# Performance work log

Hardware: AMD Instinct MI355X
Metric: run time of the kernel (lower is better)

Reference implementation:

```python
import jax, jax.numpy as jnp
import numpy as np

HID, HEADS = 2048, 16
HD = HID // HEADS  # head_dim = 128
EPS = 1e-6


def rope_tables(head_dim, max_pos, base=10000.0):
    inv = 1.0 / (base ** (jnp.arange(0, head_dim, 2, dtype=jnp.float32) / head_dim))
    t = jnp.arange(max_pos, dtype=jnp.float32)
    freqs = jnp.outer(t, inv)                      # [max_pos, d/2]
    emb = jnp.concatenate([freqs, freqs], axis=-1)  # [max_pos, d]
    return jnp.cos(emb), jnp.sin(emb)


def rotate_half(x):
    x1, x2 = jnp.split(x, 2, axis=-1)
    return jnp.concatenate([-x2, x1], axis=-1)


def lf_gate(x, c1w, c1b, c2w, c2b, rms_w):
    # x: [b, s, h]; prompt phase -> lf1/lf2 caches are zeros -> zero-pad 1 step on time axis
    xt = jnp.transpose(x, (0, 2, 1))[..., None]                 # [b, h, s, 1]
    xt = jnp.pad(xt, ((0, 0), (0, 0), (1, 0), (0, 0)))           # [b, h, s+1, 1]
    dn = ('NCHW', 'OIHW', 'NCHW')
    o1 = jax.lax.conv_general_dilated(xt, c1w, (1, 1), 'VALID', dimension_numbers=dn)
    o1 = o1 + c1b[None, :, None, None]                           # [b, h/2, s, 1]
    o1 = jnp.pad(o1, ((0, 0), (0, 0), (1, 0), (0, 0)))           # [b, h/2, s+1, 1]
    o2 = jax.lax.conv_general_dilated(o1, c2w, (1, 1), 'VALID', dimension_numbers=dn)
    o2 = o2 + c2b[None, :, None, None]                           # [b, h, s, 1]
    y = jnp.transpose(o2[..., 0], (0, 2, 1)) + x                 # residual, [b, s, h]
    var = jnp.mean(y * y, axis=-1, keepdims=True)
    return y * jax.lax.rsqrt(var + EPS) * rms_w


def setup_inputs() -> dict:
    key = jax.random.key(0)
    ks = jax.random.split(key, 10)
    b, s = 2, 2048
    inp = {
        'hidden_states': jax.random.normal(ks[0], (b, s, HID), jnp.float32),
        'positions': jnp.arange(s, dtype=jnp.int32),
        'wq': jax.random.normal(ks[1], (HID, HID), jnp.float32) * 0.02,
        'wk': jax.random.normal(ks[2], (HID, HID), jnp.float32) * 0.02,
        'wv': jax.random.normal(ks[3], (HID, HID), jnp.float32) * 0.02,
        'wo': jax.random.normal(ks[4], (HID, HID), jnp.float32) * 0.02,
        'conv1_w': jax.random.normal(ks[5], (HID // 2, HID, 2, 1), jnp.float32) * 0.02,
        'conv1_b': jnp.zeros((HID // 2,), jnp.float32),
        'conv2_w': jax.random.normal(ks[6], (HID, HID // 2, 2, 1), jnp.float32) * 0.02,
        'conv2_b': jnp.zeros((HID,), jnp.float32),
        'rms_w': jnp.ones((HID,), jnp.float32),
    }
    return inp


def reference(hidden_states, positions, wq, wk, wv, wo, conv1_w, conv1_b, conv2_w, conv2_b, rms_w):
    b, s, _ = hidden_states.shape
    # value projection from raw hidden states (pre-gate)
    v = (hidden_states @ wv).reshape(b, s, HEADS, HD)            # [b, s, H, d]
    # localized-filtering gate (prompt phase: zero caches)
    h = lf_gate(hidden_states, conv1_w, conv1_b, conv2_w, conv2_b, rms_w)
    q = h @ wq                                                   # [b, s, H*d]
    k = h @ wk
    # faithful Yuan quirk: concat q,k then reshape to [b,s,H,2d] and chunk
    qk = jnp.concatenate([q, k], axis=-1).reshape(b, s, HEADS, 2 * HD)
    q, k = jnp.split(qk, 2, axis=-1)                             # each [b, s, H, d]
    # rotary
    cos, sin = rope_tables(HD, 8192)
    c = cos[positions][None, :, None, :]                         # [1, s, 1, d]
    sn = sin[positions][None, :, None, :]
    q = q * c + rotate_half(q) * sn
    k = k * c + rotate_half(k) * sn
    # causal attention (paged attention reduces to this for the prompt)
    scale = HD ** -0.5
    scores = jnp.einsum('bqhd,bkhd->bhqk', q, k) * scale         # [b, H, s, s]
    mask = jnp.tril(jnp.ones((s, s), dtype=bool))
    scores = jnp.where(mask[None, None], scores, jnp.finfo(scores.dtype).min)
    probs = jax.nn.softmax(scores, axis=-1)
    out = jnp.einsum('bhqk,bkhd->bqhd', probs, v).reshape(b, s, HEADS * HD)
    return out @ wo
```

## Files before the change

### kernel.cpp

```cpp
#include <hip/hip_runtime.h>

#define HID 2048
#define HEADS 16
#define HD 128
#define BATCH 2
#define S 2048
#define ROWS (BATCH*S)

typedef short short8 __attribute__((ext_vector_type(8)));
typedef unsigned short ushort4v __attribute__((ext_vector_type(4)));
typedef unsigned short ushort2v __attribute__((ext_vector_type(2)));
typedef float f32x4 __attribute__((ext_vector_type(4)));
typedef __bf16 bf16x8 __attribute__((ext_vector_type(8)));
typedef __bf16 bf16x4 __attribute__((ext_vector_type(4)));

static __device__ __forceinline__ float b2f(unsigned short u) {
  union { float f; unsigned int i; } v; v.i = ((unsigned int)u) << 16; return v.f;
}
static __device__ __forceinline__ unsigned short f2b(float f) {
  union { float f; unsigned int i; } v; v.f = f;
  unsigned int u = v.i;
  unsigned int r = ((u >> 16) & 1u) + 0x7fffu;
  return (unsigned short)((u + r) >> 16);
}

static __device__ __forceinline__ void gload_lds16(const unsigned short* g, unsigned short* l) {
  __builtin_amdgcn_global_load_lds(
      (const __attribute__((address_space(1))) unsigned int*)(const void*)g,
      (__attribute__((address_space(3))) unsigned int*)(void*)l,
      16, 0, 0);
}

__global__ void fill_debug(unsigned short* __restrict__ out, long n) {
  long i = (long)blockIdx.x * blockDim.x + threadIdx.x;
  if (i < n) out[i] = 0x447A;
}

__global__ void prep_all(const float* __restrict__ c1w, const float* __restrict__ c2w,
                         const float* __restrict__ x, const int* __restrict__ positions,
                         const float* __restrict__ c1b, const float* __restrict__ c2b,
                         const float* __restrict__ rmsw,
                         unsigned short* __restrict__ w1t0, unsigned short* __restrict__ w1t1,
                         unsigned short* __restrict__ w2t0, unsigned short* __restrict__ w2t1,
                         unsigned short* __restrict__ xb,
                         float* __restrict__ ctab, float* __restrict__ stab,
                         unsigned short* __restrict__ c1bb, unsigned short* __restrict__ c2bb,
                         unsigned short* __restrict__ rmswb, unsigned short* __restrict__ zpg) {
  int job = blockIdx.y;
  if (job == 0 || job == 1) {
    const float* w = (job == 0) ? c1w : c2w;
    unsigned short* o0 = (job == 0) ? w1t0 : w2t0;
    unsigned short* o1 = (job == 0) ? w1t1 : w2t1;
    long i = (long)blockIdx.x * 256 + threadIdx.x;
    f32x4 v = *(const f32x4*)(w + i*4);
    ushort2v a = { f2b(v[0]), f2b(v[2]) };
    ushort2v b = { f2b(v[1]), f2b(v[3]) };
    *(ushort2v*)(o0 + i*2) = a;
    *(ushort2v*)(o1 + i*2) = b;
  } else if (job == 2) {
    long i = (long)blockIdx.x * 256 + threadIdx.x;
    #pragma unroll
    for (int rep = 0; rep < 2; ++rep) {
      long idx = i + (long)rep * 1048576L;
      f32x4 v = *(const f32x4*)(x + idx*4);
      ushort4v o = { f2b(v[0]), f2b(v[1]), f2b(v[2]), f2b(v[3]) };
      *(ushort4v*)(xb + idx*4) = o;
    }
  } else {
    int bx = blockIdx.x;
    if (bx < 512) {
      int t = bx * 4 + (threadIdx.x >> 6);
      int i = threadIdx.x & 63;
      float pos = (float)positions[t];
      float inv = powf(10000.0f, -(float)i / 64.0f);
      float ang = pos * inv;
      float sv, cv;
      sincosf(ang, &sv, &cv);
      ctab[t*64 + i] = cv;
      stab[t*64 + i] = sv;
    } else if (bx < 544) {
      int i = (bx - 512) * 256 + threadIdx.x;
      if (i < 1024) c1bb[i] = f2b(c1b[i]);
      if (i < 2048) { c2bb[i] = f2b(c2b[i]); rmswb[i] = f2b(rmsw[i]); }
      zpg[i] = 0;
    }
  }
}

__global__ void transpose4(const float* __restrict__ s0, const float* __restrict__ s1,
                           const float* __restrict__ s2, const float* __restrict__ s3,
                           unsigned short* __restrict__ d0, unsigned short* __restrict__ d1,
                           unsigned short* __restrict__ d2, unsigned short* __restrict__ d3) {
  __shared__ unsigned short tl[64][73];
  const float* in; unsigned short* out; int perm;
  switch (blockIdx.z) {
    case 0:  in = s0; out = d0; perm = 1; break;
    case 1:  in = s1; out = d1; perm = 1; break;
    case 2:  in = s2; out = d2; perm = 0; break;
    default: in = s3; out = d3; perm = 0; break;
  }
  int n0 = blockIdx.x * 64, k0 = blockIdx.y * 64;
  int tid = threadIdx.x;
  int r = tid >> 3, c8 = (tid & 7) * 8;
  #pragma unroll
  for (int j = 0; j < 2; ++j) {
    int rr = r + j*32;
    const float* p = in + (size_t)(k0 + rr)*HID + n0 + c8;
    f32x4 v0 = *(const f32x4*)p;
    f32x4 v1 = *(const f32x4*)(p + 4);
    #pragma unroll
    for (int e = 0; e < 4; ++e) { tl[rr][c8 + e] = f2b(v0[e]); tl[rr][c8 + 4 + e] = f2b(v1[e]); }
  }
  __syncthreads();
  #pragma unroll
  for (int j = 0; j < 2; ++j) {
    int rr = r + j*32;
    int orow = n0 + rr;
    if (perm) {
      int s5 = (orow >> 5) & 3;
      s5 = (s5 == 1) ? 2 : (s5 == 2) ? 1 : s5;
      orow = (orow & ~127) | (s5 << 5) | (orow & 31);
    }
    short8 v;
    #pragma unroll
    for (int e = 0; e < 8; ++e) v[e] = (short)tl[c8 + e][rr];
    *(short8*)(out + (size_t)orow*HID + k0 + c8) = v;
  }
}


struct SPtrs { const unsigned short* p[6]; };

static __device__ __forceinline__ void build_ptrs(SPtrs& sp,
    const unsigned short* Ap, const unsigned short* Bp, int Ksz, int sh,
    int m0, int n0, const unsigned short* zpg, int tid) {
  int lane = tid & 63;
  int scol = (((lane & 7) * 16) ^ (((lane >> 3) & 7) << 4)) >> 1;
  #pragma unroll
  for (int j = 0; j < 2; ++j) {
    int row = ((tid >> 6) * 2 + j) * 8 + (lane >> 3);
    int gr = m0 + row;
    sp.p[j]     = (sh && ((gr & (S - 1)) == 0)) ? (zpg + scol)
                                                : (Ap + (size_t)(gr - sh)*Ksz + scol);
    sp.p[2 + j] = Bp + (size_t)(n0 + row)*Ksz + scol;
    sp.p[4 + j] = Bp + (size_t)(n0 + 128 + row)*Ksz + scol;
  }
}

static __device__ __forceinline__ void stage6(unsigned short* buf, SPtrs& sp, int tid) {
  int c0 = (tid >> 6) * 1024;
  gload_lds16(sp.p[0], buf + c0);
  gload_lds16(sp.p[1], buf + c0 + 512);
  gload_lds16(sp.p[2], buf + 8192  + c0);
  gload_lds16(sp.p[3], buf + 8192  + c0 + 512);
  gload_lds16(sp.p[4], buf + 16384 + c0);
  gload_lds16(sp.p[5], buf + 16384 + c0 + 512);
  #pragma unroll
  for (int i = 0; i < 6; ++i) sp.p[i] += 64;
}

static __device__ __forceinline__ void rd_af(const unsigned short* Ah, bf16x8 (&afr)[4][2],
                                             int wm, int lr, int col0, int axor) {
  #pragma unroll
  for (int mi = 0; mi < 4; ++mi) {
    const unsigned short* rp = Ah + (wm*64 + mi*16 + lr) * 64;
    #pragma unroll
    for (int kk = 0; kk < 2; ++kk)
      afr[mi][kk] = *(const bf16x8*)(rp + (((kk*64 + col0) ^ axor) >> 1));
  }
}
static __device__ __forceinline__ void rd_bf(const unsigned short* Bh, bf16x8 (&bfr)[2][2],
                                             int wn, int lr, int col0, int axor) {
  #pragma unroll
  for (int ni = 0; ni < 2; ++ni) {
    const unsigned short* rp = Bh + (wn*32 + ni*16 + lr) * 64;
    #pragma unroll
    for (int kk = 0; kk < 2; ++kk)
      bfr[ni][kk] = *(const bf16x8*)(rp + (((kk*64 + col0) ^ axor) >> 1));
  }
}
static __device__ __forceinline__ void mfma16(const bf16x8 (&afr)[4][2], const bf16x8 (&bfr)[2][2],
                                              f32x4 (&ac)[4][2]) {
  #pragma unroll
  for (int kk = 0; kk < 2; ++kk)
    #pragma unroll
    for (int mi = 0; mi < 4; ++mi)
      #pragma unroll
      for (int ni = 0; ni < 2; ++ni)
        ac[mi][ni] = __builtin_amdgcn_mfma_f32_16x16x32_bf16(afr[mi][kk], bfr[ni][kk], ac[mi][ni], 0, 0, 0);
}

static __device__ __forceinline__ void gemm8_core(
    unsigned short* lds,
    const unsigned short* __restrict__ A1, const unsigned short* __restrict__ A2,
    const unsigned short* __restrict__ B1, const unsigned short* __restrict__ B2,
    int K1, int K2,
    const unsigned short* __restrict__ bias, const unsigned short* __restrict__ resid,
    void* __restrict__ Cout, int outmode, int N, int m0, int n0,
    int a1shift, const unsigned short* __restrict__ zrow) {
  int tid = threadIdx.x;
  int lane = tid & 63, w = tid >> 6;
  int wm = w >> 2, wn = w & 3;
  int lr = lane & 15, g = lane >> 4;
  int col0 = g * 16;
  int axor = (lr & 7) << 4;
  int nk1 = K1 >> 6;
  int nk = (K1 + K2) >> 6;
  f32x4 acc[2][4][2] = {};
  bf16x8 afr[4][2], bfr0[2][2], bfr1[2][2];

  unsigned short* buf0 = lds;
  unsigned short* buf1 = lds + 24576;
  unsigned short* buf2 = lds + 49152;

  SPtrs sp;
  build_ptrs(sp, A1, B1, K1, a1shift, m0, n0, zrow, tid);

  stage6(buf0, sp, tid);
  stage6(buf1, sp, tid);

  unsigned short* cur = buf0;
  unsigned short* nx1 = buf1;
  unsigned short* nx2 = buf2;
  for (int t = 0; t < nk; ++t) {
    if (t < nk - 1) asm volatile("s_waitcnt vmcnt(6)" ::: "memory");
    else            asm volatile("s_waitcnt vmcnt(0)" ::: "memory");
    __builtin_amdgcn_s_barrier();
    asm volatile("" ::: "memory");

    rd_af(cur,         afr,  wm, lr, col0, axor);
    rd_bf(cur + 8192,  bfr0, wn, lr, col0, axor);
    rd_bf(cur + 16384, bfr1, wn, lr, col0, axor);
    if (t + 2 < nk) {
      if (t + 2 == nk1) build_ptrs(sp, A2, B2, K2, 0, m0, n0, zrow, tid);
      stage6(nx2, sp, tid);
    }
    __builtin_amdgcn_s_setprio(1);
    mfma16(afr, bfr0, acc[0]);
    mfma16(afr, bfr1, acc[1]);
    __builtin_amdgcn_s_setprio(0);

    unsigned short* tmp = cur; cur = nx1; nx1 = nx2; nx2 = tmp;
  }

  #pragma unroll
  for (int qn = 0; qn < 2; ++qn)
    #pragma unroll
    for (int mi = 0; mi < 4; ++mi) {
      int row0 = m0 + wm*64 + mi*16 + g*4;
      #pragma unroll
      for (int ni = 0; ni < 2; ++ni) {
        int col = n0 + qn*128 + wn*32 + ni*16 + lr;
        float bv = bias ? b2f(bias[col]) : 0.f;
        f32x4 a = acc[qn][mi][ni];
        if (outmode == 3) {
          int bb = row0 >> 11;
          int s0 = row0 & (S - 1);
          size_t base = ((size_t)bb * HID + col) * S + s0;
          ushort4v pk;
          #pragma unroll
          for (int j = 0; j < 4; ++j) pk[j] = f2b(a[j]);
          *(ushort4v*)((unsigned short*)Cout + base) = pk;
        } else {
          #pragma unroll
          for (int j = 0; j < 4; ++j) {
            size_t idx = (size_t)(row0 + j) * N + col;
            float v = a[j] + bv;
            if (resid) v += b2f(resid[idx]);
            if (outmode == 1) ((float*)Cout)[idx] = v;
            else ((unsigned short*)Cout)[idx] = f2b(v);
          }
        }
      }
    }
}

template<int SHIFT>
__launch_bounds__(512, 1)
__global__ void gemm8_bt(const unsigned short* __restrict__ A1,
                         const unsigned short* __restrict__ A2,
                         const unsigned short* __restrict__ B1,
                         const unsigned short* __restrict__ B2,
                         int K1, int K2,
                         const unsigned short* __restrict__ bias,
                         const unsigned short* __restrict__ resid,
                         void* __restrict__ Cout, int outmode, int N,
                         const unsigned short* __restrict__ zrow) {
  __shared__ __align__(16) unsigned short lds[73728];
  gemm8_core(lds, A1, A2, B1, B2, K1, K2, bias, resid, Cout, outmode, N,
             blockIdx.x*128, blockIdx.y*256, SHIFT, zrow);
}

struct GemmJob {
  const unsigned short *A1, *A2, *B1, *B2;
  int K1, K2;
  const unsigned short *bias;
  void* Cout; int outmode; int N; int nby; int a1shift;
};

__launch_bounds__(512, 1)
__global__ void gemm8_dual(GemmJob j0, GemmJob j1, const unsigned short* __restrict__ zrow) {
  __shared__ __align__(16) unsigned short lds[73728];
  int by = blockIdx.y;
  GemmJob j;
  if (by < j0.nby) { j = j0; } else { j = j1; by -= j0.nby; }
  gemm8_core(lds, j.A1, j.A2, j.B1, j.B2, j.K1, j.K2, j.bias, nullptr,
             j.Cout, j.outmode, j.N, blockIdx.x*128, by*256, j.a1shift, zrow);
}

__global__ void rmsnorm_rows(const unsigned short* __restrict__ y,
                             const unsigned short* __restrict__ w,
                             unsigned short* __restrict__ out) {
  int r = blockIdx.x;
  int c8 = threadIdx.x * 8;
  const unsigned short* yr = y + (size_t)r * HID;
  short8 v = *(const short8*)(yr + c8);
  float f[8];
  float ss = 0.f;
  #pragma unroll
  for (int e = 0; e < 8; ++e) { f[e] = b2f((unsigned short)v[e]); ss += f[e]*f[e]; }
  #pragma unroll
  for (int o = 32; o; o >>= 1) ss += __shfl_xor(ss, o);
  __shared__ float red[4];
  if ((threadIdx.x & 63) == 0) red[threadIdx.x >> 6] = ss;
  __syncthreads();
  float tot = red[0] + red[1] + red[2] + red[3];
  float scale = rsqrtf(tot / (float)HID + 1e-6f);
  short8 wv = *(const short8*)(w + c8);
  short8 o8;
  #pragma unroll
  for (int e = 0; e < 8; ++e) o8[e] = (short)f2b(f[e] * scale * b2f((unsigned short)wv[e]));
  *(short8*)(out + (size_t)r*HID + c8) = o8;
}

__global__ void rope_rearrange(const unsigned short* __restrict__ qkf,
                               const float* __restrict__ ctab, const float* __restrict__ stab,
                               unsigned short* __restrict__ qr, unsigned short* __restrict__ kr) {
  int r = blockIdx.x;
  int t = r & (S - 1);
  int h = threadIdx.x >> 4;
  int i4 = (threadIdx.x & 15) * 4;
  int pc = (i4 & 31) + ((i4 >> 5) << 6);
  const unsigned short* qk = qkf + (size_t)r * (2*HID) + h * 256;
  f32x4 c = *(const f32x4*)(ctab + t*64 + i4);
  f32x4 s = *(const f32x4*)(stab + t*64 + i4);
  ushort4v q1 = *(const ushort4v*)(qk + pc);
  ushort4v q2 = *(const ushort4v*)(qk + pc + 32);
  ushort4v k1 = *(const ushort4v*)(qk + 128 + pc);
  ushort4v k2 = *(const ushort4v*)(qk + 128 + pc + 32);
  size_t o = (size_t)r * HID + (size_t)h * HD;
  const float SC = 0.08838834764831845f * 1.44269504088896340f;
  ushort4v oq1, oq2, ok1, ok2;
  #pragma unroll
  for (int e = 0; e < 4; ++e) {
    float a = b2f(q1[e]), b = b2f(q2[e]);
    float x = b2f(k1[e]), y = b2f(k2[e]);
    oq1[e] = f2b((a*c[e] - b*s[e]) * SC);
    oq2[e] = f2b((b*c[e] + a*s[e]) * SC);
    ok1[e] = f2b(x*c[e] - y*s[e]);
    ok2[e] = f2b(y*c[e] + x*s[e]);
  }
  *(ushort4v*)(qr + o + i4)      = oq1;
  *(ushort4v*)(qr + o + 64 + i4) = oq2;
  *(ushort4v*)(kr + o + i4)      = ok1;
  *(ushort4v*)(kr + o + 64 + i4) = ok2;
}

#define KT 64
#define KPK 136
#define KPV 72

__launch_bounds__(256, 3)
__global__ void attn_mfma(const unsigned short* __restrict__ Qr,
                          const unsigned short* __restrict__ Kr,
                          const unsigned short* __restrict__ Vt,
                          unsigned short* __restrict__ Out) {
  __shared__ __align__(16) unsigned short Kl[KT][KPK];
  __shared__ __align__(16) unsigned short Vl[HD][KPV];
  __shared__ __align__(16) __bf16 Pl[4][16][KPV];
  int tid = threadIdx.x, lane = tid & 63, w = tid >> 6;
  int bh = blockIdx.x;
  int b = bh >> 4, h = bh & 15;
  int qt = (int)gridDim.y - 1 - (int)blockIdx.y;
  int q0 = qt * 64;
  size_t bS = (size_t)b * S;
  size_t ho = (size_t)h * HD;
  int lr = lane & 15, g = lane >> 4;
  bf16x8 bq[4];
  {
    int qrow = q0 + w*16 + lr;
    const unsigned short* qp = Qr + (bS + qrow)*HID + ho + g*8;
    #pragma unroll
    for (int kk = 0; kk < 4; ++kk) bq[kk] = *(const bf16x8*)(qp + kk*32);
  }
  int kR = tid >> 4, kC = (tid & 15) * 8;
  int vR = tid >> 3, vC = (tid & 7) * 8;
  const unsigned short* Kg = Kr + (bS + kR)*HID + ho + kC;
  const unsigned short* Vg = Vt + ((size_t)b*HID + ho + vR)*S + vC;
  short8 kreg[4], vreg[4];
  #pragma unroll
  for (int it = 0; it < 4; ++it) {
    kreg[it] = *(const short8*)(Kg + (size_t)(it*16)*HID);
    vreg[it] = *(const short8*)(Vg + (size_t)(it*32)*S);
  }
  f32x4 o[8] = {};
  float m = -1e30f, l = 0.f;
  int ntiles = qt + 1;
  for (int kt = 0; kt < ntiles; ++kt) {
    __syncthreads();
    #pragma unroll
    for (int it = 0; it < 4; ++it) {
      *(short8*)(&Kl[it*16 + kR][kC]) = kreg[it];
      *(short8*)(&Vl[it*32 + vR][vC]) = vreg[it];
    }
    __syncthreads();
    if (kt + 1 < ntiles) {
      int k1 = (kt + 1) * KT;
      #pragma unroll
      for (int it = 0; it < 4; ++it) {
        kreg[it] = *(const short8*)(Kg + (size_t)(k1 + it*16)*HID);
        vreg[it] = *(const short8*)(Vg + (size_t)(it*32)*S + k1);
      }
    }
    f32x4 st[4] = {};
    __builtin_amdgcn_s_setprio(1);
    #pragma unroll
    for (int kk = 0; kk < 4; ++kk) {
      #pragma unroll
      for (int mi = 0; mi < 4; ++mi) {
        bf16x8 a = *(const bf16x8*)(&Kl[mi*16 + lr][kk*32 + g*8]);
        st[mi] = __builtin_amdgcn_mfma_f32_16x16x32_bf16(a, bq[kk], st[mi], 0, 0, 0);
      }
    }
    __builtin_amdgcn_s_setprio(0);
    bool lastt = (kt == ntiles - 1);
    float tm = -1e30f;
    #pragma unroll
    for (int mi = 0; mi < 4; ++mi)
      #pragma unroll
      for (int r = 0; r < 4; ++r) {
        float v = st[mi][r];
        if (lastt && (mi*16 + 4*g + r) > (w*16 + lr)) v = -1e30f;
        st[mi][r] = v;
        tm = fmaxf(tm, v);
      }
    tm = fmaxf(tm, __shfl_xor(tm, 16));
    tm = fmaxf(tm, __shfl_xor(tm, 32));
    if (!__all(tm - m <= 11.5f)) {
      float mn = fmaxf(m, tm);
      float sc = exp2f(m - mn);
      float s0 = __shfl(sc, 4*g+0), s1 = __shfl(sc, 4*g+1);
      float s2 = __shfl(sc, 4*g+2), s3 = __shfl(sc, 4*g+3);
      #pragma unroll
      for (int ni = 0; ni < 8; ++ni) {
        o[ni][0] *= s0; o[ni][1] *= s1; o[ni][2] *= s2; o[ni][3] *= s3;
      }
      l *= sc;
      m = mn;
    }
    float ts = 0.f;
    __bf16 pbf[4][4];
    #pragma unroll
    for (int mi = 0; mi < 4; ++mi)
      #pragma unroll
      for (int r = 0; r < 4; ++r) {
        float p = exp2f(st[mi][r] - m);
        ts += p;
        pbf[mi][r] = (__bf16)p;
      }
    ts += __shfl_xor(ts, 16);
    ts += __shfl_xor(ts, 32);
    l += ts;
    #pragma unroll
    for (int mi = 0; mi < 4; ++mi) {
      bf16x4 pk = { pbf[mi][0], pbf[mi][1], pbf[mi][2], pbf[mi][3] };
      *(bf16x4*)(&Pl[w][lr][mi*16 + 4*g]) = pk;
    }
    asm volatile("" ::: "memory");
    __builtin_amdgcn_s_setprio(1);
    #pragma unroll
    for (int kk = 0; kk < 2; ++kk) {
      bf16x8 a = *(const bf16x8*)(&Pl[w][lr][kk*32 + g*8]);
      #pragma unroll
      for (int ni = 0; ni < 8; ++ni) {
        bf16x8 bv = *(const bf16x8*)(&Vl[ni*16 + lr][kk*32 + g*8]);
        o[ni] = __builtin_amdgcn_mfma_f32_16x16x32_bf16(a, bv, o[ni], 0, 0, 0);
      }
    }
    __builtin_amdgcn_s_setprio(0);
  }
  float l0 = __shfl(l, 4*g+0), l1 = __shfl(l, 4*g+1);
  float l2 = __shfl(l, 4*g+2), l3 = __shfl(l, 4*g+3);
  float i0 = 1.f/l0, i1 = 1.f/l1, i2 = 1.f/l2, i3 = 1.f/l3;
  int rbase = q0 + w*16 + 4*g;
  #pragma unroll
  for (int ni = 0; ni < 8; ++ni) {
    size_t cbase = ho + ni*16 + lr;
    Out[(bS + rbase + 0)*HID + cbase] = f2b(o[ni][0]*i0);
    Out[(bS + rbase + 1)*HID + cbase] = f2b(o[ni][1]*i1);
    Out[(bS + rbase + 2)*HID + cbase] = f2b(o[ni][2]*i2);
    Out[(bS + rbase + 3)*HID + cbase] = f2b(o[ni][3]*i3);
  }
}

extern "C" void kernel_launch(void* const* d_in, const int* in_sizes, int n_in,
                              void* d_out, int out_size, void* d_ws, size_t ws_size,
                              hipStream_t stream) {
  const float* x_raw   = (const float*)d_in[0];
  const int* positions = (const int*)d_in[1];
  const float* wq_raw  = (const float*)d_in[2];
  const float* wk_raw  = (const float*)d_in[3];
  const float* wv_raw  = (const float*)d_in[4];
  const float* wo_raw  = (const float*)d_in[5];
  const float* c1w_raw = (const float*)d_in[6];
  const float* c1b_raw = (const float*)d_in[7];
  const float* c2w_raw = (const float*)d_in[8];
  const float* c2b_raw = (const float*)d_in[9];
  const float* rms_raw = (const float*)d_in[10];

  const size_t WS_NEEDED = 140000000;
  if (ws_size < WS_NEEDED) {
    long n = (long)out_size;
    fill_debug<<<dim3((unsigned)((n + 255) / 256)), dim3(256), 0, stream>>>((unsigned short*)d_out, n);
    return;
  }

  char* ws = (char*)d_ws;
  size_t off = 0;
  auto alloc = [&](size_t bytes) { char* p = ws + off; off += (bytes + 255) & ~(size_t)255; return p; };
  float* ctab          = (float*)alloc((size_t)S*64*4);
  float* stab          = (float*)alloc((size_t)S*64*4);
  unsigned short* wqkt = (unsigned short*)alloc((size_t)2*HID*HID*2);
  unsigned short* wvt  = (unsigned short*)alloc((size_t)HID*HID*2);
  unsigned short* wot  = (unsigned short*)alloc((size_t)HID*HID*2);
  unsigned short* w1t0 = (unsigned short*)alloc((size_t)1024*HID*2);
  unsigned short* w1t1 = (unsigned short*)alloc((size_t)1024*HID*2);
  unsigned short* w2t0 = (unsigned short*)alloc((size_t)HID*1024*2);
  unsigned short* w2t1 = (unsigned short*)alloc((size_t)HID*1024*2);
  unsigned short* xb   = (unsigned short*)alloc((size_t)ROWS*HID*2);
  unsigned short* qrb  = (unsigned short*)alloc((size_t)ROWS*HID*2);
  unsigned short* o1   = (unsigned short*)alloc((size_t)ROWS*1024*2);
  unsigned short* yb   = (unsigned short*)alloc((size_t)ROWS*HID*2);
  unsigned short* hg   = (unsigned short*)alloc((size_t)ROWS*HID*2);
  unsigned short* qkf  = (unsigned short*)alloc((size_t)ROWS*2*HID*2);
  unsigned short* vtg  = (unsigned short*)alloc((size_t)BATCH*HID*S*2);
  unsigned short* c1bb = (unsigned short*)alloc(1024*2);
  unsigned short* c2bb = (unsigned short*)alloc(2048*2);
  unsigned short* rmswb= (unsigned short*)alloc(2048*2);
  unsigned short* zpg  = (unsigned short*)alloc(8192*2);
  unsigned short* krr  = xb;
  unsigned short* attn = yb;

  dim3 b256(256);
  dim3 b512(512);
  prep_all<<<dim3(4096, 4), b256, 0, stream>>>(c1w_raw, c2w_raw, x_raw, positions,
                                               c1b_raw, c2b_raw, rms_raw,
                                               w1t0, w1t1, w2t0, w2t1, xb,
                                               ctab, stab, c1bb, c2bb, rmswb, zpg);
  transpose4<<<dim3(32,32,4), b256, 0, stream>>>(wq_raw, wk_raw, wv_raw, wo_raw,
                                                 wqkt, wqkt + (size_t)HID*HID, wvt, wot);
  {
    GemmJob j0 = { xb, xb, w1t0, w1t1, HID, HID, c1bb, o1, 0, 1024, 4, 1 };
    GemmJob j1 = { xb, xb, wvt,  wvt,  HID, 0,   nullptr, vtg, 3, HID, 8, 0 };
    gemm8_dual<<<dim3(ROWS/128, 12), b512, 0, stream>>>(j0, j1, zpg);
  }
  gemm8_bt<1><<<dim3(ROWS/128, HID/256), b512, 0, stream>>>(o1, o1, w2t0, w2t1, 1024, 1024, c2bb, xb, yb, 0, HID, zpg);
  rmsnorm_rows<<<dim3(ROWS), b256, 0, stream>>>(yb, rmswb, hg);
  gemm8_bt<0><<<dim3(ROWS/128, (2*HID)/256), b512, 0, stream>>>(hg, hg, wqkt, wqkt, HID, 0, nullptr, nullptr, qkf, 0, 2*HID, nullptr);
  rope_rearrange<<<dim3(ROWS), b256, 0, stream>>>(qkf, ctab, stab, qrb, krr);
  attn_mfma<<<dim3(BATCH*HEADS, S/64), b256, 0, stream>>>(qrb, krr, vtg, attn);
  gemm8_bt<0><<<dim3(ROWS/128, HID/256), b512, 0, stream>>>(attn, attn, wot, wot, HID, 0, nullptr, nullptr, d_out, 1, HID, nullptr);
}
```

Measured before the change: 368.9 us.

## Process 128 query rows per attention block and XOR-swizzle LDS tiles

The attention kernel now has each wave handle two 16-row query groups, so one block covers 128 queries. Each K/V tile loaded into LDS is reused for twice as many MFMAs, which halves K/V global traffic and per-tile sync overhead. LDS padding is replaced by an XOR swizzle to avoid bank conflicts. In exchange, register pressure roughly doubles (launch bounds drop to 2 blocks), the grid has half as many blocks, and the diagonal tile now wastes some masked work.

```diff
diff --git a/kernel.cpp b/kernel.cpp
--- a/kernel.cpp
+++ b/kernel.cpp
@@ -367,51 +367,63 @@
 }
 
 #define KT 64
-#define KPK 136
-#define KPV 72
-
-__launch_bounds__(256, 3)
+
+__launch_bounds__(256, 2)
 __global__ void attn_mfma(const unsigned short* __restrict__ Qr,
                           const unsigned short* __restrict__ Kr,
                           const unsigned short* __restrict__ Vt,
                           unsigned short* __restrict__ Out) {
-  __shared__ __align__(16) unsigned short Kl[KT][KPK];
-  __shared__ __align__(16) unsigned short Vl[HD][KPV];
-  __shared__ __align__(16) __bf16 Pl[4][16][KPV];
+  __shared__ __align__(16) unsigned short Kl[64*128];
+  __shared__ __align__(16) unsigned short Vl[128*64];
+  __shared__ __align__(16) unsigned short Pl[4*2*1024];
   int tid = threadIdx.x, lane = tid & 63, w = tid >> 6;
   int bh = blockIdx.x;
   int b = bh >> 4, h = bh & 15;
-  int qt = (int)gridDim.y - 1 - (int)blockIdx.y;
-  int q0 = qt * 64;
+  int qty = (int)gridDim.y - 1 - (int)blockIdx.y;
+  int q0 = qty * 128;
   size_t bS = (size_t)b * S;
   size_t ho = (size_t)h * HD;
   int lr = lane & 15, g = lane >> 4;
-  bf16x8 bq[4];
+  int rsw = (lr & 7) << 3;
+  bf16x8 bq0[4], bq1[4];
   {
     int qrow = q0 + w*16 + lr;
     const unsigned short* qp = Qr + (bS + qrow)*HID + ho + g*8;
     #pragma unroll
-    for (int kk = 0; kk < 4; ++kk) bq[kk] = *(const bf16x8*)(qp + kk*32);
+    for (int kk = 0; kk < 4; ++kk) {
+      bq0[kk] = *(const bf16x8*)(qp + kk*32);
+      bq1[kk] = *(const bf16x8*)(qp + (size_t)64*HID + kk*32);
+    }
   }
   int kR = tid >> 4, kC = (tid & 15) * 8;
   int vR = tid >> 3, vC = (tid & 7) * 8;
   const unsigned short* Kg = Kr + (bS + kR)*HID + ho + kC;
   const unsigned short* Vg = Vt + ((size_t)b*HID + ho + vR)*S + vC;
+  int kwo[4], vwo[4];
+  #pragma unroll
+  for (int it = 0; it < 4; ++it) {
+    int krow = it*16 + kR;
+    kwo[it] = krow*128 + (kC ^ ((krow & 7) << 3));
+    int vrow = it*32 + vR;
+    vwo[it] = vrow*64 + (vC ^ ((vrow & 7) << 3));
+  }
   short8 kreg[4], vreg[4];
   #pragma unroll
   for (int it = 0; it < 4; ++it) {
     kreg[it] = *(const short8*)(Kg + (size_t)(it*16)*HID);
     vreg[it] = *(const short8*)(Vg + (size_t)(it*32)*S);
   }
-  f32x4 o[8] = {};
-  float m = -1e30f, l = 0.f;
-  int ntiles = qt + 1;
+  f32x4 o0[8] = {}, o1[8] = {};
+  float mA = -1e30f, lA = 0.f, mB = -1e30f, lB = 0.f;
+  unsigned short* PlA = Pl + (w*2 + 0)*1024;
+  unsigned short* PlB = Pl + (w*2 + 1)*1024;
+  int ntiles = 2*qty + 2;
   for (int kt = 0; kt < ntiles; ++kt) {
     __syncthreads();
     #pragma unroll
     for (int it = 0; it < 4; ++it) {
-      *(short8*)(&Kl[it*16 + kR][kC]) = kreg[it];
-      *(short8*)(&Vl[it*32 + vR][vC]) = vreg[it];
+      *(short8*)(&Kl[kwo[it]]) = kreg[it];
+      *(short8*)(&Vl[vwo[it]]) = vreg[it];
     }
     __syncthreads();
     if (kt + 1 < ntiles) {
@@ -422,84 +434,155 @@
         vreg[it] = *(const short8*)(Vg + (size_t)(it*32)*S + k1);
       }
     }
-    f32x4 st[4] = {};
+    f32x4 st0[4] = {}, st1[4] = {};
     __builtin_amdgcn_s_setprio(1);
     #pragma unroll
     for (int kk = 0; kk < 4; ++kk) {
       #pragma unroll
       for (int mi = 0; mi < 4; ++mi) {
-        bf16x8 a = *(const bf16x8*)(&Kl[mi*16 + lr][kk*32 + g*8]);
-        st[mi] = __builtin_amdgcn_mfma_f32_16x16x32_bf16(a, bq[kk], st[mi], 0, 0, 0);
+        bf16x8 a = *(const bf16x8*)(&Kl[(mi*16 + lr)*128 + ((kk*32 + g*8) ^ rsw)]);
+        st0[mi] = __builtin_amdgcn_mfma_f32_16x16x32_bf16(a, bq0[kk], st0[mi], 0, 0, 0);
+        st1[mi] = __builtin_amdgcn_mfma_f32_16x16x32_bf16(a, bq1[kk], st1[mi], 0, 0, 0);
       }
     }
     __builtin_amdgcn_s_setprio(0);
-    bool lastt = (kt == ntiles - 1);
-    float tm = -1e30f;
-    #pragma unroll
-    for (int mi = 0; mi < 4; ++mi)
-      #pragma unroll
-      for (int r = 0; r < 4; ++r) {
-        float v = st[mi][r];
-        if (lastt && (mi*16 + 4*g + r) > (w*16 + lr)) v = -1e30f;
-        st[mi][r] = v;
-        tm = fmaxf(tm, v);
-      }
-    tm = fmaxf(tm, __shfl_xor(tm, 16));
-    tm = fmaxf(tm, __shfl_xor(tm, 32));
-    if (!__all(tm - m <= 11.5f)) {
-      float mn = fmaxf(m, tm);
-      float sc = exp2f(m - mn);
-      float s0 = __shfl(sc, 4*g+0), s1 = __shfl(sc, 4*g+1);
-      float s2 = __shfl(sc, 4*g+2), s3 = __shfl(sc, 4*g+3);
-      #pragma unroll
-      for (int ni = 0; ni < 8; ++ni) {
-        o[ni][0] *= s0; o[ni][1] *= s1; o[ni][2] *= s2; o[ni][3] *= s3;
-      }
-      l *= sc;
-      m = mn;
-    }
-    float ts = 0.f;
-    __bf16 pbf[4][4];
-    #pragma unroll
-    for (int mi = 0; mi < 4; ++mi)
-      #pragma unroll
-      for (int r = 0; r < 4; ++r) {
-        float p = exp2f(st[mi][r] - m);
-        ts += p;
-        pbf[mi][r] = (__bf16)p;
-      }
-    ts += __shfl_xor(ts, 16);
-    ts += __shfl_xor(ts, 32);
-    l += ts;
-    #pragma unroll
-    for (int mi = 0; mi < 4; ++mi) {
-      bf16x4 pk = { pbf[mi][0], pbf[mi][1], pbf[mi][2], pbf[mi][3] };
-      *(bf16x4*)(&Pl[w][lr][mi*16 + 4*g]) = pk;
+    int qloc = w*16 + lr;
+    if (kt >= ntiles - 2) {
+      int ofsA = (kt - (ntiles - 2)) * 64;
+      #pragma unroll
+      for (int mi = 0; mi < 4; ++mi)
+        #pragma unroll
+        for (int r = 0; r < 4; ++r)
+          if (mi*16 + 4*g + r + ofsA > qloc) st0[mi][r] = -1e30f;
+    }
+    if (kt == ntiles - 1) {
+      #pragma unroll
+      for (int mi = 0; mi < 4; ++mi)
+        #pragma unroll
+        for (int r = 0; r < 4; ++r)
+          if (mi*16 + 4*g + r > qloc) st1[mi][r] = -1e30f;
+    }
+    {
+      float tm = -1e30f;
+      #pragma unroll
+      for (int mi = 0; mi < 4; ++mi)
+        #pragma unroll
+        for (int r = 0; r < 4; ++r) tm = fmaxf(tm, st0[mi][r]);
+      tm = fmaxf(tm, __shfl_xor(tm, 16));
+      tm = fmaxf(tm, __shfl_xor(tm, 32));
+      if (!__all(tm - mA <= 11.5f)) {
+        float mn = fmaxf(mA, tm);
+        float sc = exp2f(mA - mn);
+        float s0 = __shfl(sc, 4*g+0), s1 = __shfl(sc, 4*g+1);
+        float s2 = __shfl(sc, 4*g+2), s3 = __shfl(sc, 4*g+3);
+        #pragma unroll
+        for (int ni = 0; ni < 8; ++ni) {
+          o0[ni][0] *= s0; o0[ni][1] *= s1; o0[ni][2] *= s2; o0[ni][3] *= s3;
+        }
+        lA *= sc;
+        mA = mn;
+      }
+      float ts = 0.f;
+      __bf16 pbf[4][4];
+      #pragma unroll
+      for (int mi = 0; mi < 4; ++mi)
+        #pragma unroll
+        for (int r = 0; r < 4; ++r) {
+          float p = exp2f(st0[mi][r] - mA);
+          ts += p;
+          pbf[mi][r] = (__bf16)p;
+        }
+      ts += __shfl_xor(ts, 16);
+      ts += __shfl_xor(ts, 32);
+      lA += ts;
+      #pragma unroll
+      for (int mi = 0; mi < 4; ++mi) {
+        bf16x4 pk = { pbf[mi][0], pbf[mi][1], pbf[mi][2], pbf[mi][3] };
+        *(bf16x4*)(&PlA[lr*64 + ((mi*16 + 4*g) ^ rsw)]) = pk;
+      }
+    }
+    {
+      float tm = -1e30f;
+      #pragma unroll
+      for (int mi = 0; mi < 4; ++mi)
+        #pragma unroll
+        for (int r = 0; r < 4; ++r) tm = fmaxf(tm, st1[mi][r]);
+      tm = fmaxf(tm, __shfl_xor(tm, 16));
+      tm = fmaxf(tm, __shfl_xor(tm, 32));
+      if (!__all(tm - mB <= 11.5f)) {
+        float mn = fmaxf(mB, tm);
+        float sc = exp2f(mB - mn);
+        float s0 = __shfl(sc, 4*g+0), s1 = __shfl(sc, 4*g+1);
+        float s2 = __shfl(sc, 4*g+2), s3 = __shfl(sc, 4*g+3);
+        #pragma unroll
+        for (int ni = 0; ni < 8; ++ni) {
+          o1[ni][0] *= s0; o1[ni][1] *= s1; o1[ni][2] *= s2; o1[ni][3] *= s3;
+        }
+        lB *= sc;
+        mB = mn;
+      }
+      float ts = 0.f;
+      __bf16 pbf[4][4];
+      #pragma unroll
+      for (int mi = 0; mi < 4; ++mi)
+        #pragma unroll
+        for (int r = 0; r < 4; ++r) {
+          float p = exp2f(st1[mi][r] - mB);
+          ts += p;
+          pbf[mi][r] = (__bf16)p;
+        }
+      ts += __shfl_xor(ts, 16);
+      ts += __shfl_xor(ts, 32);
+      lB += ts;
+      #pragma unroll
+      for (int mi = 0; mi < 4; ++mi) {
+        bf16x4 pk = { pbf[mi][0], pbf[mi][1], pbf[mi][2], pbf[mi][3] };
+        *(bf16x4*)(&PlB[lr*64 + ((mi*16 + 4*g) ^ rsw)]) = pk;
+      }
     }
     asm volatile("" ::: "memory");
     __builtin_amdgcn_s_setprio(1);
     #pragma unroll
     for (int kk = 0; kk < 2; ++kk) {
-      bf16x8 a = *(const bf16x8*)(&Pl[w][lr][kk*32 + g*8]);
+      int pc = (kk*32 + g*8) ^ rsw;
+      bf16x8 a0 = *(const bf16x8*)(&PlA[lr*64 + pc]);
+      bf16x8 a1 = *(const bf16x8*)(&PlB[lr*64 + pc]);
       #pragma unroll
       for (int ni = 0; ni < 8; ++ni) {
-        bf16x8 bv = *(const bf16x8*)(&Vl[ni*16 + lr][kk*32 + g*8]);
-        o[ni] = __builtin_amdgcn_mfma_f32_16x16x32_bf16(a, bv, o[ni], 0, 0, 0);
+        bf16x8 bv = *(const bf16x8*)(&Vl[(ni*16 + lr)*64 + pc]);
+        o0[ni] = __builtin_amdgcn_mfma_f32_16x16x32_bf16(a0, bv, o0[ni], 0, 0, 0);
+        o1[ni] = __builtin_amdgcn_mfma_f32_16x16x32_bf16(a1, bv, o1[ni], 0, 0, 0);
       }
     }
     __builtin_amdgcn_s_setprio(0);
   }
-  float l0 = __shfl(l, 4*g+0), l1 = __shfl(l, 4*g+1);
-  float l2 = __shfl(l, 4*g+2), l3 = __shfl(l, 4*g+3);
-  float i0 = 1.f/l0, i1 = 1.f/l1, i2 = 1.f/l2, i3 = 1.f/l3;
-  int rbase = q0 + w*16 + 4*g;
-  #pragma unroll
-  for (int ni = 0; ni < 8; ++ni) {
-    size_t cbase = ho + ni*16 + lr;
-    Out[(bS + rbase + 0)*HID + cbase] = f2b(o[ni][0]*i0);
-    Out[(bS + rbase + 1)*HID + cbase] = f2b(o[ni][1]*i1);
-    Out[(bS + rbase + 2)*HID + cbase] = f2b(o[ni][2]*i2);
-    Out[(bS + rbase + 3)*HID + cbase] = f2b(o[ni][3]*i3);
+  {
+    float l0 = __shfl(lA, 4*g+0), l1 = __shfl(lA, 4*g+1);
+    float l2 = __shfl(lA, 4*g+2), l3 = __shfl(lA, 4*g+3);
+    float i0 = 1.f/l0, i1 = 1.f/l1, i2 = 1.f/l2, i3 = 1.f/l3;
+    int rbase = q0 + w*16 + 4*g;
+    #pragma unroll
+    for (int ni = 0; ni < 8; ++ni) {
+      size_t cbase = ho + ni*16 + lr;
+      Out[(bS + rbase + 0)*HID + cbase] = f2b(o0[ni][0]*i0);
+      Out[(bS + rbase + 1)*HID + cbase] = f2b(o0[ni][1]*i1);
+      Out[(bS + rbase + 2)*HID + cbase] = f2b(o0[ni][2]*i2);
+      Out[(bS + rbase + 3)*HID + cbase] = f2b(o0[ni][3]*i3);
+    }
+  }
+  {
+    float l0 = __shfl(lB, 4*g+0), l1 = __shfl(lB, 4*g+1);
+    float l2 = __shfl(lB, 4*g+2), l3 = __shfl(lB, 4*g+3);
+    float i0 = 1.f/l0, i1 = 1.f/l1, i2 = 1.f/l2, i3 = 1.f/l3;
+    int rbase = q0 + 64 + w*16 + 4*g;
+    #pragma unroll
+    for (int ni = 0; ni < 8; ++ni) {
+      size_t cbase = ho + ni*16 + lr;
+      Out[(bS + rbase + 0)*HID + cbase] = f2b(o1[ni][0]*i0);
+      Out[(bS + rbase + 1)*HID + cbase] = f2b(o1[ni][1]*i1);
+      Out[(bS + rbase + 2)*HID + cbase] = f2b(o1[ni][2]*i2);
+      Out[(bS + rbase + 3)*HID + cbase] = f2b(o1[ni][3]*i3);
+    }
   }
 }
 
@@ -568,6 +651,6 @@
   rmsnorm_rows<<<dim3(ROWS), b256, 0, stream>>>(yb, rmswb, hg);
   gemm8_bt<0><<<dim3(ROWS/128, (2*HID)/256), b512, 0, stream>>>(hg, hg, wqkt, wqkt, HID, 0, nullptr, nullptr, qkf, 0, 2*HID, nullptr);
   rope_rearrange<<<dim3(ROWS), b256, 0, stream>>>(qkf, ctab, stab, qrb, krr);
-  attn_mfma<<<dim3(BATCH*HEADS, S/64), b256, 0, stream>>>(qrb, krr, vtg, attn);
+  attn_mfma<<<dim3(BATCH*HEADS, S/128), b256, 0, stream>>>(qrb, krr, vtg, attn);
   gemm8_bt<0><<<dim3(ROWS/128, HID/256), b512, 0, stream>>>(attn, attn, wot, wot, HID, 0, nullptr, nullptr, d_out, 1, HID, nullptr);
 }
```

Result: no change. 372.1 us (+0.9%).

## Double-buffer K/V tiles via direct global-to-LDS loads with XOR swizzle

Applied to the files above, without the earlier changes.

Replaces the register-staged K/V tile copy with direct global-to-LDS loads into a double-buffered shared memory area, so the next tile streams in while the current one is computed and one barrier per iteration is removed. Padded LDS rows are replaced by an XOR swizzle of column offsets to avoid bank conflicts, applied to K, V and the P scratch. LDS use rises to about 72KB per block, so the occupancy hint drops from 3 to 2 blocks per CU. A single barrier per iteration now guards both the buffer swap and the reuse of the older buffer.

```diff
diff --git a/kernel.cpp b/kernel.cpp
--- a/kernel.cpp
+++ b/kernel.cpp
@@ -367,17 +367,13 @@
 }
 
 #define KT 64
-#define KPK 136
-#define KPV 72
-
-__launch_bounds__(256, 3)
+
+__launch_bounds__(256, 2)
 __global__ void attn_mfma(const unsigned short* __restrict__ Qr,
                           const unsigned short* __restrict__ Kr,
                           const unsigned short* __restrict__ Vt,
                           unsigned short* __restrict__ Out) {
-  __shared__ __align__(16) unsigned short Kl[KT][KPK];
-  __shared__ __align__(16) unsigned short Vl[HD][KPV];
-  __shared__ __align__(16) __bf16 Pl[4][16][KPV];
+  __shared__ __align__(16) unsigned short lds[36864];
   int tid = threadIdx.x, lane = tid & 63, w = tid >> 6;
   int bh = blockIdx.x;
   int b = bh >> 4, h = bh & 15;
@@ -386,6 +382,7 @@
   size_t bS = (size_t)b * S;
   size_t ho = (size_t)h * HD;
   int lr = lane & 15, g = lane >> 4;
+  int rsw = (lr & 7) << 3;
   bf16x8 bq[4];
   {
     int qrow = q0 + w*16 + lr;
@@ -393,33 +390,45 @@
     #pragma unroll
     for (int kk = 0; kk < 4; ++kk) bq[kk] = *(const bf16x8*)(qp + kk*32);
   }
-  int kR = tid >> 4, kC = (tid & 15) * 8;
-  int vR = tid >> 3, vC = (tid & 7) * 8;
-  const unsigned short* Kg = Kr + (bS + kR)*HID + ho + kC;
-  const unsigned short* Vg = Vt + ((size_t)b*HID + ho + vR)*S + vC;
-  short8 kreg[4], vreg[4];
-  #pragma unroll
-  for (int it = 0; it < 4; ++it) {
-    kreg[it] = *(const short8*)(Kg + (size_t)(it*16)*HID);
-    vreg[it] = *(const short8*)(Vg + (size_t)(it*32)*S);
+  const unsigned short* kp[4];
+  const unsigned short* vp[4];
+  #pragma unroll
+  for (int j = 0; j < 4; ++j) {
+    int c = w*4 + j;
+    int rk = c*4 + (lane >> 4);
+    int sck = ((lane & 15) * 8) ^ ((rk & 7) << 3);
+    kp[j] = Kr + (bS + rk)*HID + ho + sck;
+    int rv = c*8 + (lane >> 3);
+    int scv = ((lane & 7) * 8) ^ ((rv & 7) << 3);
+    vp[j] = Vt + ((size_t)b*HID + ho + rv)*S + scv;
+  }
+  int cdst = (w*4) * 512;
+  unsigned short* curK = lds;
+  unsigned short* curV = lds + 8192;
+  unsigned short* nxtK = lds + 16384;
+  unsigned short* nxtV = lds + 24576;
+  #pragma unroll
+  for (int j = 0; j < 4; ++j) {
+    gload_lds16(kp[j], curK + cdst + j*512);
+    gload_lds16(vp[j], curV + cdst + j*512);
+    kp[j] += (size_t)KT * HID;
+    vp[j] += KT;
   }
   f32x4 o[8] = {};
   float m = -1e30f, l = 0.f;
+  unsigned short* PlW = lds + 32768 + w*1024;
   int ntiles = qt + 1;
   for (int kt = 0; kt < ntiles; ++kt) {
-    __syncthreads();
-    #pragma unroll
-    for (int it = 0; it < 4; ++it) {
-      *(short8*)(&Kl[it*16 + kR][kC]) = kreg[it];
-      *(short8*)(&Vl[it*32 + vR][vC]) = vreg[it];
-    }
-    __syncthreads();
+    asm volatile("s_waitcnt vmcnt(0)" ::: "memory");
+    __builtin_amdgcn_s_barrier();
+    asm volatile("" ::: "memory");
     if (kt + 1 < ntiles) {
-      int k1 = (kt + 1) * KT;
-      #pragma unroll
-      for (int it = 0; it < 4; ++it) {
-        kreg[it] = *(const short8*)(Kg + (size_t)(k1 + it*16)*HID);
-        vreg[it] = *(const short8*)(Vg + (size_t)(it*32)*S + k1);
+      #pragma unroll
+      for (int j = 0; j < 4; ++j) {
+        gload_lds16(kp[j], nxtK + cdst + j*512);
+        gload_lds16(vp[j], nxtV + cdst + j*512);
+        kp[j] += (size_t)KT * HID;
+        vp[j] += KT;
       }
     }
     f32x4 st[4] = {};
@@ -428,7 +437,7 @@
     for (int kk = 0; kk < 4; ++kk) {
       #pragma unroll
       for (int mi = 0; mi < 4; ++mi) {
-        bf16x8 a = *(const bf16x8*)(&Kl[mi*16 + lr][kk*32 + g*8]);
+        bf16x8 a = *(const bf16x8*)(&curK[(mi*16 + lr)*128 + ((kk*32 + g*8) ^ rsw)]);
         st[mi] = __builtin_amdgcn_mfma_f32_16x16x32_bf16(a, bq[kk], st[mi], 0, 0, 0);
       }
     }
@@ -474,20 +483,23 @@
     #pragma unroll
     for (int mi = 0; mi < 4; ++mi) {
       bf16x4 pk = { pbf[mi][0], pbf[mi][1], pbf[mi][2], pbf[mi][3] };
-      *(bf16x4*)(&Pl[w][lr][mi*16 + 4*g]) = pk;
+      *(bf16x4*)(&PlW[lr*64 + ((mi*16 + 4*g) ^ rsw)]) = pk;
     }
     asm volatile("" ::: "memory");
     __builtin_amdgcn_s_setprio(1);
     #pragma unroll
     for (int kk = 0; kk < 2; ++kk) {
-      bf16x8 a = *(const bf16x8*)(&Pl[w][lr][kk*32 + g*8]);
+      int pc = (kk*32 + g*8) ^ rsw;
+      bf16x8 a = *(const bf16x8*)(&PlW[lr*64 + pc]);
       #pragma unroll
       for (int ni = 0; ni < 8; ++ni) {
-        bf16x8 bv = *(const bf16x8*)(&Vl[ni*16 + lr][kk*32 + g*8]);
+        bf16x8 bv = *(const bf16x8*)(&curV[(ni*16 + lr)*64 + pc]);
         o[ni] = __builtin_amdgcn_mfma_f32_16x16x32_bf16(a, bv, o[ni], 0, 0, 0);
       }
     }
     __builtin_amdgcn_s_setprio(0);
+    unsigned short* t0 = curK; curK = nxtK; nxtK = t0;
+    unsigned short* t1 = curV; curV = nxtV; nxtV = t1;
   }
   float l0 = __shfl(l, 4*g+0), l1 = __shfl(l, 4*g+1);
   float l2 = __shfl(l, 4*g+2), l3 = __shfl(l, 4*g+3);
```

Measured after the change: 368.2 us. About the same (-0.2%).
